# Kernel tuning notes

Measured on AMD Instinct MI355X. Metric: run time of the kernel, lower is better.

The kernel has to match this reference:

```python
import jax, jax.numpy as jnp
import numpy as np

N_CELLS, IN_DIM, HID, OUT = 65536, 128, 256, 128
MLP_H = 128   # engine MLP hidden width is hard-coded to 128 in the source
N_MORPH = 32  # min(32, n_cells//4)


def setup_inputs() -> dict:
    key = jax.random.key(0)
    ks = jax.random.split(key, 18)
    s = 0.05
    return {
        "x": jax.random.normal(ks[0], (1, IN_DIM), jnp.float32),
        "hiddens": jax.random.normal(ks[1], (N_CELLS, HID), jnp.float32) * 0.1,
        "Wa1": jax.random.normal(ks[2], (MLP_H, IN_DIM + HID), jnp.float32) * s,
        "ba1": jax.random.normal(ks[3], (MLP_H,), jnp.float32) * s,
        "Wa2": jax.random.normal(ks[4], (OUT, MLP_H), jnp.float32) * s,
        "ba2": jax.random.normal(ks[5], (OUT,), jnp.float32) * s,
        "Wg1": jax.random.normal(ks[6], (MLP_H, IN_DIM + HID), jnp.float32) * s,
        "bg1": jax.random.normal(ks[7], (MLP_H,), jnp.float32) * s,
        "Wg2": jax.random.normal(ks[8], (OUT, MLP_H), jnp.float32) * s,
        "bg2": jax.random.normal(ks[9], (OUT,), jnp.float32) * s,
        "W_ih": jax.random.normal(ks[10], (3 * HID, OUT + 1), jnp.float32) * s,
        "W_hh": jax.random.normal(ks[11], (3 * HID, HID), jnp.float32) * s,
        "b_ih": jax.random.normal(ks[12], (3 * HID,), jnp.float32) * s,
        "b_hh": jax.random.normal(ks[13], (3 * HID,), jnp.float32) * s,
        "nat_w": jnp.eye(HID, dtype=jnp.float32),  # nn.init.eye_
        "morph_w": jax.random.normal(ks[14], (N_MORPH, HID, HID), jnp.float32) * 0.02,
        "morph_src": jax.random.randint(ks[15], (N_MORPH,), 0, N_CELLS, jnp.int32),
        "morph_tgt": jax.random.randint(ks[16], (N_MORPH,), 0, N_CELLS, jnp.int32),
        "step": 0,
    }


def _forward(x, hiddens, Wa1, ba1, Wa2, ba2, Wg1, bg1, Wg2, bg2,
             W_ih, W_hh, b_ih, b_hh, nat_w, morph_w, morph_src, morph_tgt, step):
    n = hiddens.shape[0]
    # --- BenchMind, batched over all cells (x broadcast to every cell) ---
    xb = jnp.broadcast_to(x, (n, x.shape[-1]))
    combined = jnp.concatenate([xb, hiddens], axis=-1)               # [n, in+hid]
    a = jax.nn.relu(combined @ Wa1.T + ba1) @ Wa2.T + ba2            # [n, out]
    g = jax.nn.relu(combined @ Wg1.T + bg1) @ Wg2.T + bg2            # [n, out]
    out = a - g                                                       # [n, out]
    tension = jnp.mean(out * out, axis=-1, keepdims=True)            # [n, 1]
    # mem_input is detached in torch
    mem_in = jax.lax.stop_gradient(jnp.concatenate([out, tension], axis=-1))
    # --- PyTorch GRUCell math ---
    gi = mem_in @ W_ih.T + b_ih                                      # [n, 3H]
    gh = hiddens @ W_hh.T + b_hh                                     # [n, 3H]
    i_r, i_z, i_n = jnp.split(gi, 3, axis=-1)
    h_r, h_z, h_n = jnp.split(gh, 3, axis=-1)
    r = jax.nn.sigmoid(i_r + h_r)
    z = jax.nn.sigmoid(i_z + h_z)
    nn_ = jnp.tanh(i_n + r * h_n)
    hid = jax.lax.stop_gradient((1.0 - z) * nn_ + z * hiddens)       # detached new hiddens
    if step % 3 == 0:
        hid = jax.lax.stop_gradient(hid @ nat_w.T)                   # natural transformation
    # --- limit / colimit (morphism gather-transform-aggregate) ---
    limit = jnp.einsum('mij,mj->i', morph_w, hid[morph_src]) / N_MORPH
    colimit = jnp.einsum('mji,mj->i', morph_w, hid[morph_tgt]) / N_MORPH
    diff = limit - colimit
    cat_tension = jnp.mean(diff * diff)
    hid = hid + 0.05 * jax.lax.stop_gradient(diff)[None, :]
    # --- faction sync (+ debate if step > 5) ---
    n_f = min(8, n // 2)
    fs = n // n_f
    hf = hid[: n_f * fs].reshape(n_f, fs, hid.shape[-1])
    fmean = hf.mean(axis=1, keepdims=True)                           # [n_f,1,H]
    hf = 0.85 * hf + 0.15 * fmean
    if step > 5:
        global_op = hf.mean(axis=1).mean(axis=0)                     # mean of faction means
        dc = max(1, fs // 4)
        hf = hf.at[:, :dc].set(0.85 * hf[:, :dc] + 0.15 * global_op)
    hid = jnp.concatenate([hf.reshape(n_f * fs, -1), hid[n_f * fs:]], axis=0)
    # --- tension-weighted combination (weights detached: .item() in torch) ---
    t = jax.lax.stop_gradient(tension[:, 0])                         # [n]
    w = jax.nn.softmax(t, axis=0)
    combined_out = jnp.sum(w[:, None] * out, axis=0, keepdims=True)  # [1, out]
    avg_tension = jnp.mean(tension) + 0.1 * cat_tension
    return combined_out, avg_tension, hid


def reference(x, hiddens, Wa1, ba1, Wa2, ba2, Wg1, bg1, Wg2, bg2,
              W_ih, W_hh, b_ih, b_hh, nat_w, morph_w, morph_src, morph_tgt, step):
    combined_out, avg_tension, _ = _forward(
        x, hiddens, Wa1, ba1, Wa2, ba2, Wg1, bg1, Wg2, bg2,
        W_ih, W_hh, b_ih, b_hh, nat_w, morph_w, morph_src, morph_tgt, step)
    return combined_out, avg_tension
```

## Files before the change

### kernel.cpp

```cpp
#include <hip/hip_runtime.h>
#include <math.h>

#define N_CELLS 65536

#define OFF_W1B   0
#define OFF_W2A   32768
#define OFF_XW1B  49152
#define OFF_B2D   49408
#define OFF_PT    49536
#define OFF_PE    50560
#define OFF_POUT  51584
#define OFF_MI4   182656
#define OFF_TEN   190848
#define OFF_HH4   190912
#define OFF_GI    207296
#define OFF_GH    256448
#define OFF_PLIM  305600
#define OFF_PCOL  313792

typedef short bf16x8 __attribute__((ext_vector_type(8)));
typedef float f32x4  __attribute__((ext_vector_type(4)));

__device__ __forceinline__ unsigned short f2bf(float f) {
    unsigned u = __builtin_bit_cast(unsigned, f);
    u += 0x7FFFu + ((u >> 16) & 1u);
    return (unsigned short)(u >> 16);
}

__global__ __launch_bounds__(256) void k_prep(
    const float* __restrict__ x, const float* __restrict__ hiddens,
    const float* __restrict__ Wa1, const float* __restrict__ ba1,
    const float* __restrict__ Wa2, const float* __restrict__ ba2,
    const float* __restrict__ Wg1, const float* __restrict__ bg1,
    const float* __restrict__ Wg2, const float* __restrict__ bg2,
    const int* __restrict__ msrc, const int* __restrict__ mtgt,
    float* __restrict__ ws)
{
    const int b = blockIdx.x, t = threadIdx.x;
    unsigned short* w1b = (unsigned short*)(ws + OFF_W1B);
    unsigned short* w2a = (unsigned short*)(ws + OFF_W2A);
    if (b < 256) {
        const int n = b;
        const float* row = (n < 128) ? &Wa1[n * 384] : &Wg1[(n - 128) * 384];
        const int sk = ((t >> 5) * 4 + ((t >> 3) & 3));
        w1b[(sk * 256 + n) * 8 + (t & 7)] = f2bf(row[128 + t]);
        if (n < 128) {
            float w2 = (t < 128) ? Wa2[n * 128 + t] : -Wg2[n * 128 + (t - 128)];
            w2a[(sk * 128 + n) * 8 + (t & 7)] = f2bf(w2);
        }
    } else if (b == 256) {
        const int n = t;
        const float* wr = (n < 128) ? &Wa1[n * 384] : &Wg1[(n - 128) * 384];
        float s = (n < 128) ? ba1[n] : bg1[n - 128];
        for (int j = 0; j < 128; ++j) s = fmaf(x[j], wr[j], s);
        ws[OFF_XW1B + n] = s;
        if (n < 128) ws[OFF_B2D + n] = ba2[n] - bg2[n];
    } else {
        for (int g = 0; g < 64; ++g) {
            const int cell = (g < 32) ? msrc[g] : mtgt[g - 32];
            ws[OFF_HH4 + (t >> 2) * 256 + g * 4 + (t & 3)] = hiddens[(size_t)cell * 256 + t];
        }
    }
}

__global__ __launch_bounds__(512, 4) void k_main(
    const float* __restrict__ hiddens,
    const int* __restrict__ msrc, const int* __restrict__ mtgt,
    float* __restrict__ ws)
{
    __shared__ __align__(16) char smem[81920];
    short* hA  = (short*)&smem[0];
    short* h1A = (short*)&smem[32768];
    short* wbf = (short*)&smem[65536];

    const int tid  = threadIdx.x;
    const int lane = tid & 63;
    const int wid  = tid >> 6;
    const int wn   = wid >> 1;
    const int wc   = wid & 1;
    const int l15  = lane & 15;
    const int l4   = lane >> 4;
    const int blk  = blockIdx.x;
    const int cell0 = blk * 64;

    for (int it = 0; it < 4; ++it) {
        const int idx = it * 512 + tid;
        const int c = idx >> 5, q = idx & 31;
        const float4* src = (const float4*)(hiddens + (size_t)(cell0 + c) * 256 + q * 8);
        float4 va = src[0], vb = src[1];
        bf16x8 bv;
        bv[0] = (short)f2bf(va.x); bv[1] = (short)f2bf(va.y);
        bv[2] = (short)f2bf(va.z); bv[3] = (short)f2bf(va.w);
        bv[4] = (short)f2bf(vb.x); bv[5] = (short)f2bf(vb.y);
        bv[6] = (short)f2bf(vb.z); bv[7] = (short)f2bf(vb.w);
        const int slot = (c & 48) | ((c ^ q) & 15);
        *(bf16x8*)&hA[(q * 64 + slot) * 8] = bv;
    }

    const uint4* w1g = (const uint4*)(ws + OFF_W1B);
    const uint4* w2g = (const uint4*)(ws + OFF_W2A);
    f32x4 acc[4][2];
#pragma unroll
    for (int nt = 0; nt < 4; ++nt)
#pragma unroll
        for (int ct = 0; ct < 2; ++ct) acc[nt][ct] = (f32x4)0.f;

    uint4 wr0 = w1g[tid], wr1 = w1g[512 + tid];
    for (int s = 0; s < 8; ++s) {
        __syncthreads();
        ((uint4*)wbf)[tid] = wr0; ((uint4*)wbf)[512 + tid] = wr1;
        __syncthreads();
        if (s < 7) { wr0 = w1g[(s + 1) * 1024 + tid]; wr1 = w1g[(s + 1) * 1024 + 512 + tid]; }
        else       { wr0 = w2g[tid]; }
        const int kcg = s * 4 + l4;
        bf16x8 afr[4], bfr[2];
#pragma unroll
        for (int nt = 0; nt < 4; ++nt)
            afr[nt] = *(const bf16x8*)&wbf[(l4 * 256 + wn * 64 + nt * 16 + l15) * 8];
#pragma unroll
        for (int ct = 0; ct < 2; ++ct) {
            const int slot = (wc * 32 + ct * 16) | ((l15 ^ kcg) & 15);
            bfr[ct] = *(const bf16x8*)&hA[(kcg * 64 + slot) * 8];
        }
#pragma unroll
        for (int nt = 0; nt < 4; ++nt)
#pragma unroll
            for (int ct = 0; ct < 2; ++ct)
                acc[nt][ct] = __builtin_amdgcn_mfma_f32_16x16x32_bf16(afr[nt], bfr[ct], acc[nt][ct], 0, 0, 0);
    }

#pragma unroll
    for (int nt = 0; nt < 4; ++nt) {
#pragma unroll
        for (int r = 0; r < 4; ++r) {
            const int n = wn * 64 + nt * 16 + l4 * 4 + r;
            const float xb = ws[OFF_XW1B + n];
            const int kc2 = n >> 3, j2 = n & 7;
#pragma unroll
            for (int ct = 0; ct < 2; ++ct) {
                const int c = wc * 32 + ct * 16 + l15;
                float v = fmaxf(acc[nt][ct][r] + xb, 0.f);
                const int slot = (c & 48) | ((c ^ kc2) & 15);
                h1A[(kc2 * 64 + slot) * 8 + j2] = (short)f2bf(v);
            }
        }
    }

    f32x4 acc2[2][2];
#pragma unroll
    for (int ot = 0; ot < 2; ++ot)
#pragma unroll
        for (int ct = 0; ct < 2; ++ct) acc2[ot][ct] = (f32x4)0.f;

    for (int s = 0; s < 8; ++s) {
        __syncthreads();
        ((uint4*)wbf)[tid] = wr0;
        __syncthreads();
        if (s < 7) wr0 = w2g[(s + 1) * 512 + tid];
        const int kcg = s * 4 + l4;
        bf16x8 afr2[2], bfr2[2];
#pragma unroll
        for (int ot = 0; ot < 2; ++ot)
            afr2[ot] = *(const bf16x8*)&wbf[(l4 * 128 + wn * 32 + ot * 16 + l15) * 8];
#pragma unroll
        for (int ct = 0; ct < 2; ++ct) {
            const int slot = (wc * 32 + ct * 16) | ((l15 ^ kcg) & 15);
            bfr2[ct] = *(const bf16x8*)&h1A[(kcg * 64 + slot) * 8];
        }
#pragma unroll
        for (int ot = 0; ot < 2; ++ot)
#pragma unroll
            for (int ct = 0; ct < 2; ++ct)
                acc2[ot][ct] = __builtin_amdgcn_mfma_f32_16x16x32_bf16(afr2[ot], bfr2[ct], acc2[ot][ct], 0, 0, 0);
    }

    float outv[2][2][4];
#pragma unroll
    for (int ot = 0; ot < 2; ++ot)
#pragma unroll
        for (int r = 0; r < 4; ++r) {
            const int o = wn * 32 + ot * 16 + l4 * 4 + r;
            const float bd = ws[OFF_B2D + o];
#pragma unroll
            for (int ct = 0; ct < 2; ++ct)
                outv[ot][ct][r] = acc2[ot][ct][r] + bd;
        }
    __syncthreads();

    float* out_sm = (float*)smem;
    float* part   = (float*)&smem[65536];
    float* e_sm   = (float*)&smem[65536 + 1024];
    float* t_sm   = (float*)&smem[65536 + 1280];

#pragma unroll
    for (int ot = 0; ot < 2; ++ot)
#pragma unroll
        for (int ct = 0; ct < 2; ++ct) {
            const int c = wc * 32 + ct * 16 + l15;
#pragma unroll
            for (int r = 0; r < 4; ++r) {
                const int o = wn * 32 + ot * 16 + l4 * 4 + r;
                out_sm[c * 130 + o] = outv[ot][ct][r];
            }
        }
#pragma unroll
    for (int ct = 0; ct < 2; ++ct) {
        float sq = 0.f;
#pragma unroll
        for (int ot = 0; ot < 2; ++ot)
#pragma unroll
            for (int r = 0; r < 4; ++r) sq = fmaf(outv[ot][ct][r], outv[ot][ct][r], sq);
        sq += __shfl_xor(sq, 16);
        sq += __shfl_xor(sq, 32);
        if (l4 == 0) part[wn * 64 + wc * 32 + ct * 16 + l15] = sq;
    }
    __syncthreads();

    if (tid < 64) {
        const float tv = (part[tid] + part[64 + tid] + part[128 + tid] + part[192 + tid]) * (1.f / 128.f);
        const float ev = expf(tv);
        t_sm[tid] = tv; e_sm[tid] = ev;
        float pt = tv, pe = ev;
        for (int off = 32; off > 0; off >>= 1) {
            pt += __shfl_down(pt, off);
            pe += __shfl_down(pe, off);
        }
        if (tid == 0) { ws[OFF_PT + blk] = pt; ws[OFF_PE + blk] = pe; }
    }
    __syncthreads();

    if (tid < 128) {
        float s = 0.f;
        for (int c = 0; c < 64; ++c) s = fmaf(e_sm[c], out_sm[c * 130 + tid], s);
        ws[OFF_POUT + blk * 128 + tid] = s;
    } else if (tid < 192) {
        const int g = tid - 128;
        const int cell = (g < 32) ? msrc[g] : mtgt[g - 32];
        if ((cell >> 6) == blk) {
            const int c = cell & 63;
            for (int o = 0; o < 128; ++o)
                ws[OFF_MI4 + (o >> 2) * 256 + g * 4 + (o & 3)] = out_sm[c * 130 + o];
            ws[OFF_TEN + g] = t_sm[c];
        }
    }
}

__global__ __launch_bounds__(256) void k_tail1(
    const float* __restrict__ W_ih, const float* __restrict__ W_hh,
    const float* __restrict__ b_ih, const float* __restrict__ b_hh,
    float* __restrict__ ws)
{
    const int lane = threadIdx.x & 63;
    const int w    = threadIdx.x >> 6;
    const int row  = __builtin_amdgcn_readfirstlane(blockIdx.x * 4 + w);
    const float* mi4 = ws + OFF_MI4;
    const float* hh4 = ws + OFF_HH4;

    const float* wi = W_ih + row * 129;
    float gi = b_ih[row];
#pragma unroll 8
    for (int q = 0; q < 32; ++q) {
        float4 a = *(const float4*)(mi4 + q * 256 + lane * 4);
        gi = fmaf(wi[4 * q + 0], a.x, gi);
        gi = fmaf(wi[4 * q + 1], a.y, gi);
        gi = fmaf(wi[4 * q + 2], a.z, gi);
        gi = fmaf(wi[4 * q + 3], a.w, gi);
    }
    gi = fmaf(ws[OFF_TEN + lane], wi[128], gi);

    const float* wh = W_hh + (size_t)row * 256;
    float gh = b_hh[row];
#pragma unroll 8
    for (int q = 0; q < 64; ++q) {
        float4 a = *(const float4*)(hh4 + q * 256 + lane * 4);
        float4 b = *(const float4*)(wh + 4 * q);
        gh = fmaf(b.x, a.x, gh);
        gh = fmaf(b.y, a.y, gh);
        gh = fmaf(b.z, a.z, gh);
        gh = fmaf(b.w, a.w, gh);
    }
    ws[OFF_GI + row * 64 + lane] = gi;
    ws[OFF_GH + row * 64 + lane] = gh;
}

__global__ __launch_bounds__(512) void k_tail2(
    const float* __restrict__ nat_w, const float* __restrict__ morph_w,
    const int* __restrict__ step, float* __restrict__ ws)
{
    __shared__ float hd[2][256];
    __shared__ float hn[2][256];
    const int tid = threadIdx.x, half = tid >> 8, t = tid & 255, m = blockIdx.x;
    const int g = half * 32 + m;

    const float i_r = ws[OFF_GI + (0 * 256 + t) * 64 + g];
    const float i_z = ws[OFF_GI + (1 * 256 + t) * 64 + g];
    const float i_n = ws[OFF_GI + (2 * 256 + t) * 64 + g];
    const float h_r = ws[OFF_GH + (0 * 256 + t) * 64 + g];
    const float h_z = ws[OFF_GH + (1 * 256 + t) * 64 + g];
    const float h_n = ws[OFF_GH + (2 * 256 + t) * 64 + g];
    const float hv  = ws[OFF_HH4 + (t >> 2) * 256 + g * 4 + (t & 3)];

    const float r  = 1.f / (1.f + expf(-(i_r + h_r)));
    const float z  = 1.f / (1.f + expf(-(i_z + h_z)));
    const float nn = tanhf(i_n + r * h_n);
    const float hid = (1.f - z) * nn + z * hv;

    hd[half][t] = hid;
    __syncthreads();
    if (step[0] % 3 == 0) {
        const float4* wr = (const float4*)(nat_w + (size_t)t * 256);
        float s = 0.f;
        for (int q = 0; q < 64; ++q) {
            float4 wq = wr[q];
            s = fmaf(wq.x, hd[half][4 * q + 0], s);
            s = fmaf(wq.y, hd[half][4 * q + 1], s);
            s = fmaf(wq.z, hd[half][4 * q + 2], s);
            s = fmaf(wq.w, hd[half][4 * q + 3], s);
        }
        hn[half][t] = s;
    } else {
        hn[half][t] = hid;
    }
    __syncthreads();

    const float* wm = morph_w + (size_t)m * 65536;
    if (half == 0) {
        const float4* r_ = (const float4*)(wm + (size_t)t * 256);
        float L = 0.f;
        for (int q = 0; q < 64; ++q) {
            float4 wq = r_[q];
            L = fmaf(wq.x, hn[0][4 * q + 0], L);
            L = fmaf(wq.y, hn[0][4 * q + 1], L);
            L = fmaf(wq.z, hn[0][4 * q + 2], L);
            L = fmaf(wq.w, hn[0][4 * q + 3], L);
        }
        ws[OFF_PLIM + m * 256 + t] = L;
    } else {
        float C = 0.f;
        for (int j = 0; j < 256; ++j)
            C = fmaf(wm[j * 256 + t], hn[1][j], C);
        ws[OFF_PCOL + m * 256 + t] = C;
    }
}

__global__ __launch_bounds__(256) void k_out(const float* __restrict__ ws,
                                             float* __restrict__ out)
{
    __shared__ float red[256];
    const int b = blockIdx.x, t = threadIdx.x;
    if (b < 128) {
        float so = 0.f, se = 0.f;
        for (int i = t; i < 1024; i += 256) {
            so += ws[OFF_POUT + i * 128 + b];
            se += ws[OFF_PE + i];
        }
        red[t] = so; __syncthreads();
        for (int s = 128; s > 0; s >>= 1) { if (t < s) red[t] += red[t + s]; __syncthreads(); }
        const float SO = red[0]; __syncthreads();
        red[t] = se; __syncthreads();
        for (int s = 128; s > 0; s >>= 1) { if (t < s) red[t] += red[t + s]; __syncthreads(); }
        if (t == 0) out[b] = SO / red[0];
    } else {
        float pt = 0.f;
        for (int i = t; i < 1024; i += 256) pt += ws[OFF_PT + i];
        float L = 0.f, C = 0.f;
        for (int m = 0; m < 32; ++m) {
            L += ws[OFF_PLIM + m * 256 + t];
            C += ws[OFF_PCOL + m * 256 + t];
        }
        const float d = (L - C) * (1.f / 32.f);
        red[t] = d * d; __syncthreads();
        for (int s = 128; s > 0; s >>= 1) { if (t < s) red[t] += red[t + s]; __syncthreads(); }
        const float cat = red[0] * (1.f / 256.f); __syncthreads();
        red[t] = pt; __syncthreads();
        for (int s = 128; s > 0; s >>= 1) { if (t < s) red[t] += red[t + s]; __syncthreads(); }
        if (t == 0) out[128] = red[0] * (1.f / 65536.f) + 0.1f * cat;
    }
}

extern "C" void kernel_launch(void* const* d_in, const int* in_sizes, int n_in,
                              void* d_out, int out_size, void* d_ws, size_t ws_size,
                              hipStream_t stream)
{
    const float* x     = (const float*)d_in[0];
    const float* hidd  = (const float*)d_in[1];
    const float* Wa1   = (const float*)d_in[2];
    const float* ba1   = (const float*)d_in[3];
    const float* Wa2   = (const float*)d_in[4];
    const float* ba2   = (const float*)d_in[5];
    const float* Wg1   = (const float*)d_in[6];
    const float* bg1   = (const float*)d_in[7];
    const float* Wg2   = (const float*)d_in[8];
    const float* bg2   = (const float*)d_in[9];
    const float* W_ih  = (const float*)d_in[10];
    const float* W_hh  = (const float*)d_in[11];
    const float* b_ih  = (const float*)d_in[12];
    const float* b_hh  = (const float*)d_in[13];
    const float* nat_w = (const float*)d_in[14];
    const float* mw    = (const float*)d_in[15];
    const int*   msrc  = (const int*)d_in[16];
    const int*   mtgt  = (const int*)d_in[17];
    const int*   step  = (const int*)d_in[18];

    float* out = (float*)d_out;
    float* ws  = (float*)d_ws;

    k_prep <<<258, 256, 0, stream>>>(x, hidd, Wa1, ba1, Wa2, ba2, Wg1, bg1, Wg2, bg2, msrc, mtgt, ws);
    k_main <<<1024, 512, 0, stream>>>(hidd, msrc, mtgt, ws);
    k_tail1<<<192, 256, 0, stream>>>(W_ih, W_hh, b_ih, b_hh, ws);
    k_tail2<<<32, 512, 0, stream>>>(nat_w, mw, step, ws);
    k_out  <<<129, 256, 0, stream>>>(ws, out);
}
```

Baseline: 83.01 us.

## Split fused MLP into two GEMM kernels with resident W1 and bf16 intermediate

The fused main kernel is split in two. k_g1 keeps the whole bf16 first-layer weight resident in shared memory across 256 cells per block and streams hiddens from global into registers with a prefetch, then writes the ReLU activations as bf16 to a workspace buffer. k_g2 holds the second-layer weights in registers and reads those activations straight from global. This removes the per-block restaging of weights through LDS and the barriers that went with it, at the cost of an extra kernel launch and a round trip of 32 MB of intermediate data through global memory. The k_prep hidden-row gather is spread over 64 blocks, and the partial-output layout is transposed so the final reduction reads coalesced.

```diff
diff --git a/kernel.cpp b/kernel.cpp
--- a/kernel.cpp
+++ b/kernel.cpp
@@ -17,14 +17,25 @@
 #define OFF_GH    256448
 #define OFF_PLIM  305600
 #define OFF_PCOL  313792
+#define OFF_H1F   4194304
 
 typedef short bf16x8 __attribute__((ext_vector_type(8)));
+typedef short s16x4  __attribute__((ext_vector_type(4)));
 typedef float f32x4  __attribute__((ext_vector_type(4)));
 
 __device__ __forceinline__ unsigned short f2bf(float f) {
     unsigned u = __builtin_bit_cast(unsigned, f);
     u += 0x7FFFu + ((u >> 16) & 1u);
     return (unsigned short)(u >> 16);
+}
+
+__device__ __forceinline__ bf16x8 cvt8(float4 a, float4 b) {
+    bf16x8 v;
+    v[0] = (short)f2bf(a.x); v[1] = (short)f2bf(a.y);
+    v[2] = (short)f2bf(a.z); v[3] = (short)f2bf(a.w);
+    v[4] = (short)f2bf(b.x); v[5] = (short)f2bf(b.y);
+    v[6] = (short)f2bf(b.z); v[7] = (short)f2bf(b.w);
+    return v;
 }
 
 __global__ __launch_bounds__(256) void k_prep(
@@ -42,7 +53,7 @@
     if (b < 256) {
         const int n = b;
         const float* row = (n < 128) ? &Wa1[n * 384] : &Wg1[(n - 128) * 384];
-        const int sk = ((t >> 5) * 4 + ((t >> 3) & 3));
+        const int sk = t >> 3;
         w1b[(sk * 256 + n) * 8 + (t & 7)] = f2bf(row[128 + t]);
         if (n < 128) {
             float w2 = (t < 128) ? Wa2[n * 128 + t] : -Wg2[n * 128 + (t - 128)];
@@ -56,141 +67,138 @@
         ws[OFF_XW1B + n] = s;
         if (n < 128) ws[OFF_B2D + n] = ba2[n] - bg2[n];
     } else {
-        for (int g = 0; g < 64; ++g) {
-            const int cell = (g < 32) ? msrc[g] : mtgt[g - 32];
-            ws[OFF_HH4 + (t >> 2) * 256 + g * 4 + (t & 3)] = hiddens[(size_t)cell * 256 + t];
-        }
-    }
-}
-
-__global__ __launch_bounds__(512, 4) void k_main(
-    const float* __restrict__ hiddens,
+        const int g = b - 257;
+        const int cell = (g < 32) ? msrc[g] : mtgt[g - 32];
+        ws[OFF_HH4 + (t >> 2) * 256 + g * 4 + (t & 3)] = hiddens[(size_t)cell * 256 + t];
+    }
+}
+
+__global__ __launch_bounds__(1024, 4) void k_g1(
+    const float* __restrict__ hiddens, float* __restrict__ ws)
+{
+    __shared__ __align__(16) short w1[65536];
+    const int tid = threadIdx.x;
+    {
+        const uint4* src = (const uint4*)(ws + OFF_W1B);
+        uint4* dst = (uint4*)w1;
+#pragma unroll
+        for (int i = 0; i < 8; ++i) dst[i * 1024 + tid] = src[i * 1024 + tid];
+    }
+    __syncthreads();
+
+    const int lane = tid & 63, wid = tid >> 6;
+    const int wn = wid & 3, wc = wid >> 2;
+    const int l15 = lane & 15, l4 = lane >> 4;
+
+    float4 xb[4];
+#pragma unroll
+    for (int nt = 0; nt < 4; ++nt)
+        xb[nt] = *(const float4*)(ws + OFF_XW1B + wn * 64 + nt * 16 + l4 * 4);
+
+    unsigned short* h1 = (unsigned short*)(ws + OFF_H1F);
+    const float* hbase = hiddens + (size_t)(blockIdx.x * 256 + wc * 16 + l15) * 256;
+
+    float4 A0, B0, A1, B1;
+    { const float* p = hbase + l4 * 8;                 A0 = *(const float4*)p; B0 = *(const float4*)(p + 4); }
+    { const float* p = hbase + 32 + l4 * 8;            A1 = *(const float4*)p; B1 = *(const float4*)(p + 4); }
+
+    for (int t = 0; t < 4; ++t) {
+        f32x4 acc[4];
+#pragma unroll
+        for (int nt = 0; nt < 4; ++nt) acc[nt] = (f32x4)0.f;
+
+#pragma unroll
+        for (int s = 0; s < 8; ++s) {
+            bf16x8 bfr = cvt8(A0, B0);
+            A0 = A1; B0 = B1;
+            const int g = t * 8 + s + 2;
+            if (g < 32) {
+                const float* p = hbase + (g >> 3) * 16384 + (g & 7) * 32 + l4 * 8;
+                A1 = *(const float4*)p; B1 = *(const float4*)(p + 4);
+            }
+#pragma unroll
+            for (int nt = 0; nt < 4; ++nt) {
+                bf16x8 afr = *(const bf16x8*)&w1[((s * 4 + l4) * 256 + wn * 64 + nt * 16 + l15) * 8];
+                acc[nt] = __builtin_amdgcn_mfma_f32_16x16x32_bf16(afr, bfr, acc[nt], 0, 0, 0);
+            }
+        }
+        unsigned short* hrow = h1 + (size_t)(blockIdx.x * 256 + t * 64 + wc * 16 + l15) * 256;
+#pragma unroll
+        for (int nt = 0; nt < 4; ++nt) {
+            s16x4 pk;
+            pk[0] = (short)f2bf(fmaxf(acc[nt][0] + xb[nt].x, 0.f));
+            pk[1] = (short)f2bf(fmaxf(acc[nt][1] + xb[nt].y, 0.f));
+            pk[2] = (short)f2bf(fmaxf(acc[nt][2] + xb[nt].z, 0.f));
+            pk[3] = (short)f2bf(fmaxf(acc[nt][3] + xb[nt].w, 0.f));
+            *(s16x4*)&hrow[wn * 64 + nt * 16 + l4 * 4] = pk;
+        }
+    }
+}
+
+__global__ __launch_bounds__(512, 4) void k_g2(
     const int* __restrict__ msrc, const int* __restrict__ mtgt,
     float* __restrict__ ws)
 {
-    __shared__ __align__(16) char smem[81920];
-    short* hA  = (short*)&smem[0];
-    short* h1A = (short*)&smem[32768];
-    short* wbf = (short*)&smem[65536];
-
-    const int tid  = threadIdx.x;
-    const int lane = tid & 63;
-    const int wid  = tid >> 6;
-    const int wn   = wid >> 1;
-    const int wc   = wid & 1;
-    const int l15  = lane & 15;
-    const int l4   = lane >> 4;
-    const int blk  = blockIdx.x;
-    const int cell0 = blk * 64;
-
-    for (int it = 0; it < 4; ++it) {
-        const int idx = it * 512 + tid;
-        const int c = idx >> 5, q = idx & 31;
-        const float4* src = (const float4*)(hiddens + (size_t)(cell0 + c) * 256 + q * 8);
-        float4 va = src[0], vb = src[1];
-        bf16x8 bv;
-        bv[0] = (short)f2bf(va.x); bv[1] = (short)f2bf(va.y);
-        bv[2] = (short)f2bf(va.z); bv[3] = (short)f2bf(va.w);
-        bv[4] = (short)f2bf(vb.x); bv[5] = (short)f2bf(vb.y);
-        bv[6] = (short)f2bf(vb.z); bv[7] = (short)f2bf(vb.w);
-        const int slot = (c & 48) | ((c ^ q) & 15);
-        *(bf16x8*)&hA[(q * 64 + slot) * 8] = bv;
-    }
-
-    const uint4* w1g = (const uint4*)(ws + OFF_W1B);
+    __shared__ float out_sm[64 * 130];
+    __shared__ float part[256];
+    __shared__ float e_sm[64];
+    __shared__ float t_sm[64];
+
+    const int tid = threadIdx.x;
+    const int lane = tid & 63, wid = tid >> 6;
+    const int wn = wid >> 1, wc = wid & 1;
+    const int l15 = lane & 15, l4 = lane >> 4;
+    const int blk = blockIdx.x;
+
     const uint4* w2g = (const uint4*)(ws + OFF_W2A);
-    f32x4 acc[4][2];
-#pragma unroll
-    for (int nt = 0; nt < 4; ++nt)
-#pragma unroll
-        for (int ct = 0; ct < 2; ++ct) acc[nt][ct] = (f32x4)0.f;
-
-    uint4 wr0 = w1g[tid], wr1 = w1g[512 + tid];
+    uint4 a2[8][2];
+#pragma unroll
+    for (int s = 0; s < 8; ++s)
+#pragma unroll
+        for (int ot = 0; ot < 2; ++ot)
+            a2[s][ot] = w2g[(s * 4 + l4) * 128 + wn * 32 + ot * 16 + l15];
+
+    const unsigned short* h1 = (const unsigned short*)(ws + OFF_H1F);
+    const unsigned short* hr[2];
+#pragma unroll
+    for (int ct = 0; ct < 2; ++ct)
+        hr[ct] = h1 + (size_t)(blk * 64 + wc * 32 + ct * 16 + l15) * 256;
+
+    f32x4 acc2[2][2];
+#pragma unroll
+    for (int ot = 0; ot < 2; ++ot)
+#pragma unroll
+        for (int ct = 0; ct < 2; ++ct) acc2[ot][ct] = (f32x4)0.f;
+
+    uint4 pb0 = *(const uint4*)&hr[0][l4 * 8];
+    uint4 pb1 = *(const uint4*)&hr[1][l4 * 8];
+#pragma unroll
     for (int s = 0; s < 8; ++s) {
-        __syncthreads();
-        ((uint4*)wbf)[tid] = wr0; ((uint4*)wbf)[512 + tid] = wr1;
-        __syncthreads();
-        if (s < 7) { wr0 = w1g[(s + 1) * 1024 + tid]; wr1 = w1g[(s + 1) * 1024 + 512 + tid]; }
-        else       { wr0 = w2g[tid]; }
-        const int kcg = s * 4 + l4;
-        bf16x8 afr[4], bfr[2];
-#pragma unroll
-        for (int nt = 0; nt < 4; ++nt)
-            afr[nt] = *(const bf16x8*)&wbf[(l4 * 256 + wn * 64 + nt * 16 + l15) * 8];
-#pragma unroll
-        for (int ct = 0; ct < 2; ++ct) {
-            const int slot = (wc * 32 + ct * 16) | ((l15 ^ kcg) & 15);
-            bfr[ct] = *(const bf16x8*)&hA[(kcg * 64 + slot) * 8];
-        }
-#pragma unroll
-        for (int nt = 0; nt < 4; ++nt)
-#pragma unroll
-            for (int ct = 0; ct < 2; ++ct)
-                acc[nt][ct] = __builtin_amdgcn_mfma_f32_16x16x32_bf16(afr[nt], bfr[ct], acc[nt][ct], 0, 0, 0);
-    }
-
-#pragma unroll
-    for (int nt = 0; nt < 4; ++nt) {
-#pragma unroll
-        for (int r = 0; r < 4; ++r) {
-            const int n = wn * 64 + nt * 16 + l4 * 4 + r;
-            const float xb = ws[OFF_XW1B + n];
-            const int kc2 = n >> 3, j2 = n & 7;
-#pragma unroll
-            for (int ct = 0; ct < 2; ++ct) {
-                const int c = wc * 32 + ct * 16 + l15;
-                float v = fmaxf(acc[nt][ct][r] + xb, 0.f);
-                const int slot = (c & 48) | ((c ^ kc2) & 15);
-                h1A[(kc2 * 64 + slot) * 8 + j2] = (short)f2bf(v);
-            }
-        }
-    }
-
-    f32x4 acc2[2][2];
-#pragma unroll
-    for (int ot = 0; ot < 2; ++ot)
-#pragma unroll
-        for (int ct = 0; ct < 2; ++ct) acc2[ot][ct] = (f32x4)0.f;
-
-    for (int s = 0; s < 8; ++s) {
-        __syncthreads();
-        ((uint4*)wbf)[tid] = wr0;
-        __syncthreads();
-        if (s < 7) wr0 = w2g[(s + 1) * 512 + tid];
-        const int kcg = s * 4 + l4;
-        bf16x8 afr2[2], bfr2[2];
-#pragma unroll
-        for (int ot = 0; ot < 2; ++ot)
-            afr2[ot] = *(const bf16x8*)&wbf[(l4 * 128 + wn * 32 + ot * 16 + l15) * 8];
-#pragma unroll
-        for (int ct = 0; ct < 2; ++ct) {
-            const int slot = (wc * 32 + ct * 16) | ((l15 ^ kcg) & 15);
-            bfr2[ct] = *(const bf16x8*)&h1A[(kcg * 64 + slot) * 8];
-        }
-#pragma unroll
-        for (int ot = 0; ot < 2; ++ot)
-#pragma unroll
-            for (int ct = 0; ct < 2; ++ct)
-                acc2[ot][ct] = __builtin_amdgcn_mfma_f32_16x16x32_bf16(afr2[ot], bfr2[ct], acc2[ot][ct], 0, 0, 0);
+        bf16x8 bfr0 = __builtin_bit_cast(bf16x8, pb0);
+        bf16x8 bfr1 = __builtin_bit_cast(bf16x8, pb1);
+        if (s < 7) {
+            pb0 = *(const uint4*)&hr[0][(s + 1) * 32 + l4 * 8];
+            pb1 = *(const uint4*)&hr[1][(s + 1) * 32 + l4 * 8];
+        }
+#pragma unroll
+        for (int ot = 0; ot < 2; ++ot) {
+            bf16x8 af = __builtin_bit_cast(bf16x8, a2[s][ot]);
+            acc2[ot][0] = __builtin_amdgcn_mfma_f32_16x16x32_bf16(af, bfr0, acc2[ot][0], 0, 0, 0);
+            acc2[ot][1] = __builtin_amdgcn_mfma_f32_16x16x32_bf16(af, bfr1, acc2[ot][1], 0, 0, 0);
+        }
     }
 
     float outv[2][2][4];
 #pragma unroll
-    for (int ot = 0; ot < 2; ++ot)
-#pragma unroll
-        for (int r = 0; r < 4; ++r) {
-            const int o = wn * 32 + ot * 16 + l4 * 4 + r;
-            const float bd = ws[OFF_B2D + o];
-#pragma unroll
-            for (int ct = 0; ct < 2; ++ct)
-                outv[ot][ct][r] = acc2[ot][ct][r] + bd;
-        }
-    __syncthreads();
-
-    float* out_sm = (float*)smem;
-    float* part   = (float*)&smem[65536];
-    float* e_sm   = (float*)&smem[65536 + 1024];
-    float* t_sm   = (float*)&smem[65536 + 1280];
+    for (int ot = 0; ot < 2; ++ot) {
+        float4 bd = *(const float4*)(ws + OFF_B2D + wn * 32 + ot * 16 + l4 * 4);
+        const float bv[4] = {bd.x, bd.y, bd.z, bd.w};
+#pragma unroll
+        for (int ct = 0; ct < 2; ++ct)
+#pragma unroll
+            for (int r = 0; r < 4; ++r)
+                outv[ot][ct][r] = acc2[ot][ct][r] + bv[r];
+    }
 
 #pragma unroll
     for (int ot = 0; ot < 2; ++ot)
@@ -198,10 +206,8 @@
         for (int ct = 0; ct < 2; ++ct) {
             const int c = wc * 32 + ct * 16 + l15;
 #pragma unroll
-            for (int r = 0; r < 4; ++r) {
-                const int o = wn * 32 + ot * 16 + l4 * 4 + r;
-                out_sm[c * 130 + o] = outv[ot][ct][r];
-            }
+            for (int r = 0; r < 4; ++r)
+                out_sm[c * 130 + wn * 32 + ot * 16 + l4 * 4 + r] = outv[ot][ct][r];
         }
 #pragma unroll
     for (int ct = 0; ct < 2; ++ct) {
@@ -232,7 +238,7 @@
     if (tid < 128) {
         float s = 0.f;
         for (int c = 0; c < 64; ++c) s = fmaf(e_sm[c], out_sm[c * 130 + tid], s);
-        ws[OFF_POUT + blk * 128 + tid] = s;
+        ws[OFF_POUT + tid * 1024 + blk] = s;
     } else if (tid < 192) {
         const int g = tid - 128;
         const int cell = (g < 32) ? msrc[g] : mtgt[g - 32];
@@ -351,7 +357,7 @@
     if (b < 128) {
         float so = 0.f, se = 0.f;
         for (int i = t; i < 1024; i += 256) {
-            so += ws[OFF_POUT + i * 128 + b];
+            so += ws[OFF_POUT + b * 1024 + i];
             se += ws[OFF_PE + i];
         }
         red[t] = so; __syncthreads();
@@ -405,8 +411,9 @@
     float* out = (float*)d_out;
     float* ws  = (float*)d_ws;
 
-    k_prep <<<258, 256, 0, stream>>>(x, hidd, Wa1, ba1, Wa2, ba2, Wg1, bg1, Wg2, bg2, msrc, mtgt, ws);
-    k_main <<<1024, 512, 0, stream>>>(hidd, msrc, mtgt, ws);
+    k_prep <<<321, 256, 0, stream>>>(x, hidd, Wa1, ba1, Wa2, ba2, Wg1, bg1, Wg2, bg2, msrc, mtgt, ws);
+    k_g1   <<<256, 1024, 0, stream>>>(hidd, ws);
+    k_g2   <<<1024, 512, 0, stream>>>(msrc, mtgt, ws);
     k_tail1<<<192, 256, 0, stream>>>(W_ih, W_hh, b_ih, b_hh, ws);
     k_tail2<<<32, 512, 0, stream>>>(nat_w, mw, step, ws);
     k_out  <<<129, 256, 0, stream>>>(ws, out);
```

Result: slower. 141.9 us (+70.9%).
